# Kernel tuning notes

Measured on AMD Instinct MI355X. Metric: run time of the kernel, lower is better.

The kernel has to match this reference:

```python
import jax, jax.numpy as jnp
import numpy as np

N_NODES = 50000
N_EDGES = 1_250_000
D = 64
L = 3

def setup_inputs() -> dict:
    key = jax.random.key(0)
    k1, k2, k3, k4, k5, k6 = jax.random.split(key, 6)
    h = jax.random.normal(k1, (N_NODES, D), dtype=jnp.float32)
    edge_weight = jax.random.uniform(k2, (N_EDGES,), dtype=jnp.float32)
    # Glorot-ish scale keeps tanh in its responsive range
    Ws = jax.random.normal(k3, (L, D, D), dtype=jnp.float32) * (1.0 / np.sqrt(D))
    bs = jax.random.normal(k4, (L, D), dtype=jnp.float32) * 0.01
    src = jax.random.randint(k5, (N_EDGES,), 0, N_NODES, dtype=jnp.int64 if jax.config.jax_enable_x64 else jnp.int32)
    dst = jax.random.randint(k6, (N_EDGES,), 0, N_NODES, dtype=jnp.int64 if jax.config.jax_enable_x64 else jnp.int32)
    return {"h": h, "edge_weight": edge_weight, "Ws": Ws, "bs": bs, "src": src, "dst": dst}

def reference(h, edge_weight, Ws, bs, src, dst):
    # Stacked DGL GraphConv(norm='none'), edge-weighted: aggregate-then-transform
    # (in_feats == out_feats, so DGL aggregates first), tanh between layers,
    # concat of all intermediate representations along feature dim.
    n = h.shape[0]
    results = [h]
    for i in range(L):
        msg = h[src] * edge_weight[:, None]            # [E, D] gather-scale
        agg = jax.ops.segment_sum(msg, dst, num_segments=n)  # [N, D] scatter-add
        h = agg @ Ws[i] + bs[i]                        # dense transform + bias
        if i != L - 1:
            h = jnp.tanh(h)
        results.append(h)
    return jnp.concatenate(results, axis=1)           # [N, (L+1)*D]
```

## Files before the change

kernel.cpp:

```cpp
#include <hip/hip_runtime.h>
#include <hip/hip_fp16.h>
#include <math.h>

#define N_NODES 50000
#define N_EDGES 1250000
#define D 64
#define OUTC 256
#define CAP 64
#define SCAN_BLOCKS ((N_NODES + 255) / 256)

#define WSB_CNT      0
#define WSB_BUCKET   802816
#define WSB_H16_0    13602816
#define WSB_H16_1    20002816
#define WS_BUCKET_NEEDED 26402816

#define WS_DEG      0
#define WS_FILL     204800
#define WS_ROWPTR   409600
#define WS_BSUM     609664
#define WS_BOFF     610496
#define WS_EDGES    614400
#define WS_H16_0    10616832
#define WS_H16_1    (WS_H16_0 + (size_t)N_NODES * D * 2)
#define WS_F16_NEEDED (WS_H16_1 + (size_t)N_NODES * D * 2)
#define WS_CSR_NEEDED (WS_EDGES + (size_t)N_EDGES * 8)


#define PREP_T (50000 + 800000)
__global__ __launch_bounds__(256) void prep_kernel(const float* __restrict__ h,
                                                   float* __restrict__ out,
                                                   __half* __restrict__ h16,
                                                   int4* __restrict__ cnt4) {
    int tid = blockIdx.x * 256 + threadIdx.x;
    if (tid < 50000) { cnt4[tid] = make_int4(0, 0, 0, 0); return; }
    tid -= 50000;
    if (tid >= 800000) return;
    int row = tid >> 4;
    int c4  = tid & 15;
    float4 v = ((const float4*)h)[tid];
    ((float4*)(out + (size_t)row * OUTC))[c4] = v;
    __half2* p = (__half2*)(h16 + (size_t)row * D + c4 * 4);
    p[0] = __floats2half2_rn(v.x, v.y);
    p[1] = __floats2half2_rn(v.z, v.w);
}

#define FILL_GBLK 611
__global__ __launch_bounds__(256) void bucket_fill_kernel(const int* __restrict__ src,
                                                          const int* __restrict__ dst,
                                                          const float* __restrict__ ew,
                                                          int* __restrict__ cnt,
                                                          unsigned* __restrict__ bucket) {
    int p = blockIdx.x & 7;
    int g = blockIdx.x >> 3;
    int nlo = p * 6250, nhi = nlo + 6250;
    int e0 = (g * 256 + threadIdx.x) * 8;
    if (e0 >= N_EDGES) return;
    int4   d0 = *(const int4*)(dst + e0);
    int4   d1 = *(const int4*)(dst + e0 + 4);
    int4   s0 = *(const int4*)(src + e0);
    int4   s1 = *(const int4*)(src + e0 + 4);
    float4 w0 = *(const float4*)(ew + e0);
    float4 w1 = *(const float4*)(ew + e0 + 4);
    int   dd[8] = {d0.x, d0.y, d0.z, d0.w, d1.x, d1.y, d1.z, d1.w};
    int   ss[8] = {s0.x, s0.y, s0.z, s0.w, s1.x, s1.y, s1.z, s1.w};
    float ww[8] = {w0.x, w0.y, w0.z, w0.w, w1.x, w1.y, w1.z, w1.w};
#pragma unroll
    for (int i = 0; i < 8; i++) {
        int d = dd[i];
        if (d >= nlo && d < nhi) {
            int c = atomicAdd(&cnt[d * 4], 1) & (CAP - 1);
            unsigned hw = (unsigned)__half_as_ushort(__float2half(ww[i]));
            bucket[(size_t)d * CAP + c] = ((unsigned)ss[i] << 16) | hw;
        }
    }
}

#define LAYER5_BLOCKS 12500
__device__ __forceinline__ float rdlane(float v, int l) {
    return __int_as_float(__builtin_amdgcn_readlane(__float_as_int(v), l));
}
__global__ __launch_bounds__(256) void layer5_kernel(const __half* __restrict__ h16src,
                                                     const unsigned* __restrict__ bucket,
                                                     const int* __restrict__ cnt,
                                                     const float* __restrict__ W,
                                                     const float* __restrict__ bias,
                                                     float* __restrict__ hout,
                                                     __half* __restrict__ h16out,
                                                     int apply_tanh) {
    int t = threadIdx.x, lane = t & 63, wv = t >> 6;
    int fb = lane & 7;
    int eo = lane >> 3;
    const uint4* __restrict__ h4 = (const uint4*)h16src;
    float bv = bias[lane];

    int n  = __builtin_amdgcn_readfirstlane(blockIdx.x * 4 + wv);
    int cn = cnt[n * 4];
    const uint4* bp4 = (const uint4*)(bucket + (size_t)n * CAP);
    uint4 qqa = bp4[eo];
    cn = __builtin_amdgcn_readfirstlane(cn > CAP ? CAP : cn);
    int off2 = (cn > 32) ? 8 : 0;
    uint4 qqb = bp4[off2 + eo];

    float Wreg[D];
#pragma unroll
    for (int k = 0; k < D; k++) Wreg[k] = W[k * D + lane];

    float acc[8];
#pragma unroll
    for (int u = 0; u < 8; u++) acc[u] = 0.0f;

    auto processChunk = [&](uint4 qq, int j) {
        int sbase = j + eo * 4;
        unsigned ee[4];
        ee[0] = (sbase + 0 < cn) ? qq.x : 0u;
        ee[1] = (sbase + 1 < cn) ? qq.y : 0u;
        ee[2] = (sbase + 2 < cn) ? qq.z : 0u;
        ee[3] = (sbase + 3 < cn) ? qq.w : 0u;
        uint4 g[4];
#pragma unroll
        for (int i = 0; i < 4; i++)
            g[i] = h4[(size_t)(ee[i] >> 16) * 8 + fb];
#pragma unroll
        for (int i = 0; i < 4; i++) {
            float w = __half2float(__ushort_as_half((unsigned short)(ee[i] & 0xFFFFu)));
            const __half2* hv = (const __half2*)&g[i];
#pragma unroll
            for (int tt = 0; tt < 4; tt++) {
                float2 f = __half22float2(hv[tt]);
                acc[2 * tt]     = fmaf(f.x, w, acc[2 * tt]);
                acc[2 * tt + 1] = fmaf(f.y, w, acc[2 * tt + 1]);
            }
        }
    };

    processChunk(qqa, 0);
    if (cn > 32) processChunk(qqb, 32);

#pragma unroll
    for (int u = 0; u < 8; u++) {
        acc[u] += __shfl_xor(acc[u], 8);
        acc[u] += __shfl_xor(acc[u], 16);
        acc[u] += __shfl_xor(acc[u], 32);
    }

    float o0 = bv, o1 = 0.f, o2 = 0.f, o3 = 0.f;
#pragma unroll
    for (int k = 0; k < D; k += 4) {
        o0 = fmaf(rdlane(acc[(k + 0) & 7], (k + 0) >> 3), Wreg[k + 0], o0);
        o1 = fmaf(rdlane(acc[(k + 1) & 7], (k + 1) >> 3), Wreg[k + 1], o1);
        o2 = fmaf(rdlane(acc[(k + 2) & 7], (k + 2) >> 3), Wreg[k + 2], o2);
        o3 = fmaf(rdlane(acc[(k + 3) & 7], (k + 3) >> 3), Wreg[k + 3], o3);
    }
    float o = (o0 + o1) + (o2 + o3);
    if (apply_tanh) o = tanhf(o);
    hout[(size_t)n * OUTC + lane] = o;
    if (h16out) h16out[(size_t)n * D + lane] = __float2half(o);
}


__global__ __launch_bounds__(256) void copy_h_kernel(const float* __restrict__ h,
                                                     float* __restrict__ out,
                                                     __half* __restrict__ h16) {
    int idx = blockIdx.x * 256 + threadIdx.x;
    if (idx >= N_NODES * D / 4) return;
    int row = idx >> 4;
    int c4  = idx & 15;
    float4 v = ((const float4*)h)[idx];
    ((float4*)(out + (size_t)row * OUTC))[c4] = v;
    if (h16) {
        __half2* p = (__half2*)(h16 + (size_t)row * D + c4 * 4);
        p[0] = __floats2half2_rn(v.x, v.y);
        p[1] = __floats2half2_rn(v.z, v.w);
    }
}

__global__ __launch_bounds__(256) void hist_kernel(const int* __restrict__ dst,
                                                   int* __restrict__ deg) {
    int e = blockIdx.x * 256 + threadIdx.x;
    if (e >= N_EDGES) return;
    atomicAdd(&deg[dst[e]], 1);
}

__global__ __launch_bounds__(256) void scan_partial_kernel(const int* __restrict__ deg,
                                                           int* __restrict__ bsum) {
    __shared__ int ws4[4];
    int t = threadIdx.x;
    int i = blockIdx.x * 256 + t;
    int v = (i < N_NODES) ? deg[i] : 0;
#pragma unroll
    for (int off = 32; off >= 1; off >>= 1) v += __shfl_xor(v, off);
    if ((t & 63) == 0) ws4[t >> 6] = v;
    __syncthreads();
    if (t == 0) bsum[blockIdx.x] = ws4[0] + ws4[1] + ws4[2] + ws4[3];
}

__global__ __launch_bounds__(256) void scan_bsum_kernel(const int* __restrict__ bsum,
                                                        int* __restrict__ boff,
                                                        int* __restrict__ row_ptr) {
    __shared__ int wsum[4];
    int t = threadIdx.x, lane = t & 63, w = t >> 6;
    int v = (t < SCAN_BLOCKS) ? bsum[t] : 0;
    int x = v;
#pragma unroll
    for (int off = 1; off < 64; off <<= 1) {
        int y = __shfl_up(x, off);
        if (lane >= off) x += y;
    }
    if (lane == 63) wsum[w] = x;
    __syncthreads();
    int wo = 0;
    for (int u = 0; u < w; u++) wo += wsum[u];
    int excl = wo + x - v;
    if (t < SCAN_BLOCKS) boff[t] = excl;
    if (t == SCAN_BLOCKS - 1) row_ptr[N_NODES] = excl + v;
}

__global__ __launch_bounds__(256) void scan_final_kernel(const int* __restrict__ deg,
                                                         const int* __restrict__ boff,
                                                         int* __restrict__ row_ptr) {
    __shared__ int wsum[4];
    int t = threadIdx.x, lane = t & 63, w = t >> 6;
    int i = blockIdx.x * 256 + t;
    int v = (i < N_NODES) ? deg[i] : 0;
    int x = v;
#pragma unroll
    for (int off = 1; off < 64; off <<= 1) {
        int y = __shfl_up(x, off);
        if (lane >= off) x += y;
    }
    if (lane == 63) wsum[w] = x;
    __syncthreads();
    int wo = 0;
    for (int u = 0; u < w; u++) wo += wsum[u];
    if (i < N_NODES) row_ptr[i] = boff[blockIdx.x] + wo + (x - v);
}

__global__ __launch_bounds__(256) void fill_kernel(const int* __restrict__ src,
                                                   const int* __restrict__ dst,
                                                   const float* __restrict__ ew,
                                                   const int* __restrict__ row_ptr,
                                                   int* __restrict__ fill,
                                                   int2* __restrict__ edges) {
    int e = blockIdx.x * 256 + threadIdx.x;
    if (e >= N_EDGES) return;
    int d = dst[e];
    int p = atomicAdd(&fill[d], 1);
    edges[row_ptr[d] + p] = make_int2(src[e], __float_as_int(ew[e]));
}

#define LAYER_BLOCKS 3125
__global__ __launch_bounds__(256) void layer2_kernel(const __half* __restrict__ h16src,
                                                     const int2* __restrict__ edges,
                                                     const int* __restrict__ row_ptr,
                                                     const float* __restrict__ W,
                                                     const float* __restrict__ bias,
                                                     float* __restrict__ hout,
                                                     __half* __restrict__ h16out,
                                                     int apply_tanh) {
    __shared__ float Wlds[D * D];
    int t = threadIdx.x, lane = t & 63, wv = t >> 6;
    for (int i = t; i < D * D; i += 256) Wlds[i] = W[i];
    __syncthreads();
    int p  = lane & 31;
    int hh = lane >> 5;
    const __half2* __restrict__ h2 = (const __half2*)h16src;
    float bv = bias[lane];
    int waveId = blockIdx.x * 4 + wv;
    for (int n0 = waveId; n0 < N_NODES; n0 += LAYER_BLOCKS * 4) {
        int n = __builtin_amdgcn_readfirstlane(n0);
        int beg = __builtin_amdgcn_readfirstlane(row_ptr[n]);
        int end = __builtin_amdgcn_readfirstlane(row_ptr[n + 1]);
        float2 acc = make_float2(0.0f, 0.0f);
        int j = beg;
        for (; j + 8 <= end; j += 8) {
            int2 a0 = edges[j + 0], a1 = edges[j + 1];
            int2 a2 = edges[j + 2], a3 = edges[j + 3];
            int2 a4 = edges[j + 4], a5 = edges[j + 5];
            int2 a6 = edges[j + 6], a7 = edges[j + 7];
            int   s0 = hh ? a1.x : a0.x;  float w0 = __int_as_float(hh ? a1.y : a0.y);
            int   s1 = hh ? a3.x : a2.x;  float w1 = __int_as_float(hh ? a3.y : a2.y);
            int   s2 = hh ? a5.x : a4.x;  float w2 = __int_as_float(hh ? a5.y : a4.y);
            int   s3 = hh ? a7.x : a6.x;  float w3 = __int_as_float(hh ? a7.y : a6.y);
            __half2 v0 = h2[(size_t)s0 * 32 + p];
            __half2 v1 = h2[(size_t)s1 * 32 + p];
            __half2 v2 = h2[(size_t)s2 * 32 + p];
            __half2 v3 = h2[(size_t)s3 * 32 + p];
            acc.x = fmaf(__low2float(v0), w0, acc.x);  acc.y = fmaf(__high2float(v0), w0, acc.y);
            acc.x = fmaf(__low2float(v1), w1, acc.x);  acc.y = fmaf(__high2float(v1), w1, acc.y);
            acc.x = fmaf(__low2float(v2), w2, acc.x);  acc.y = fmaf(__high2float(v2), w2, acc.y);
            acc.x = fmaf(__low2float(v3), w3, acc.x);  acc.y = fmaf(__high2float(v3), w3, acc.y);
        }
        for (; j + 2 <= end; j += 2) {
            int2 a0 = edges[j], a1 = edges[j + 1];
            int   s0 = hh ? a1.x : a0.x;  float w0 = __int_as_float(hh ? a1.y : a0.y);
            __half2 v0 = h2[(size_t)s0 * 32 + p];
            acc.x = fmaf(__low2float(v0), w0, acc.x);  acc.y = fmaf(__high2float(v0), w0, acc.y);
        }
        if (j < end) {
            int2 a0 = edges[j];
            float w0 = hh ? 0.0f : __int_as_float(a0.y);
            __half2 v0 = h2[(size_t)a0.x * 32 + p];
            acc.x = fmaf(__low2float(v0), w0, acc.x);  acc.y = fmaf(__high2float(v0), w0, acc.y);
        }
        acc.x += __shfl_xor(acc.x, 32);
        acc.y += __shfl_xor(acc.y, 32);
        float o0 = bv, o1 = 0.f, o2 = 0.f, o3 = 0.f;
#pragma unroll
        for (int k = 0; k < D; k += 4) {
            int q = k >> 1;
            o0 = fmaf(__shfl(acc.x, q),     Wlds[(k + 0) * D + lane], o0);
            o1 = fmaf(__shfl(acc.y, q),     Wlds[(k + 1) * D + lane], o1);
            o2 = fmaf(__shfl(acc.x, q + 1), Wlds[(k + 2) * D + lane], o2);
            o3 = fmaf(__shfl(acc.y, q + 1), Wlds[(k + 3) * D + lane], o3);
        }
        float o = (o0 + o1) + (o2 + o3);
        if (apply_tanh) o = tanhf(o);
        hout[(size_t)n * OUTC + lane] = o;
        if (h16out) h16out[(size_t)n * D + lane] = __float2half(o);
    }
}

__global__ __launch_bounds__(256) void scatter_kernel(const float* __restrict__ hin,
                                                      const float* __restrict__ ew,
                                                      const int* __restrict__ src,
                                                      const int* __restrict__ dst,
                                                      float* __restrict__ agg) {
    long long gid = (long long)blockIdx.x * 256 + threadIdx.x;
    int e = (int)(gid >> 6);
    int lane = (int)(gid & 63);
    if (e >= N_EDGES) return;
    float v = hin[(size_t)src[e] * OUTC + lane] * ew[e];
    atomicAdd(&agg[(size_t)dst[e] * OUTC + lane], v);
}

__global__ __launch_bounds__(256) void gemm_kernel(float* __restrict__ hio,
                                                   const float* __restrict__ W,
                                                   const float* __restrict__ bias,
                                                   int apply_tanh) {
    __shared__ float Wl[D][D + 1];
    __shared__ float rowbuf[4][D];
    int t = threadIdx.x;
    for (int i = t; i < D * D; i += 256) Wl[i >> 6][i & (D - 1)] = W[i];
    int r = t >> 6, c = t & (D - 1);
    float bv = bias[c];
    int row0 = blockIdx.x * 64;
    for (int rr = 0; rr < 64; rr += 4) {
        int row = row0 + rr + r;
        __syncthreads();
        rowbuf[r][c] = (row < N_NODES) ? hio[(size_t)row * OUTC + c] : 0.0f;
        __syncthreads();
        float acc = bv;
#pragma unroll
        for (int k = 0; k < D; k++) acc = fmaf(rowbuf[r][k], Wl[k][c], acc);
        if (apply_tanh) acc = tanhf(acc);
        if (row < N_NODES) hio[(size_t)row * OUTC + c] = acc;
    }
}

extern "C" void kernel_launch(void* const* d_in, const int* in_sizes, int n_in,
                              void* d_out, int out_size, void* d_ws, size_t ws_size,
                              hipStream_t stream) {
    const float* h   = (const float*)d_in[0];
    const float* ew  = (const float*)d_in[1];
    const float* Ws  = (const float*)d_in[2];
    const float* bs  = (const float*)d_in[3];
    const int*   src = (const int*)d_in[4];
    const int*   dst = (const int*)d_in[5];
    float* out = (float*)d_out;

    if (ws_size >= WS_BUCKET_NEEDED) {
        char* ws = (char*)d_ws;
        int*      cnt    = (int*)(ws + WSB_CNT);
        unsigned* bucket = (unsigned*)(ws + WSB_BUCKET);
        __half*   h16a   = (__half*)(ws + WSB_H16_0);
        __half*   h16b   = (__half*)(ws + WSB_H16_1);

        prep_kernel<<<(PREP_T + 255) / 256, 256, 0, stream>>>(
            h, out, h16a, (int4*)cnt);
        bucket_fill_kernel<<<FILL_GBLK * 8, 256, 0, stream>>>(
            src, dst, ew, cnt, bucket);
        for (int i = 0; i < 3; i++) {
            float* hout = out + (size_t)(i + 1) * D;
            __half* hsrc = (i & 1) ? h16b : h16a;
            __half* hdst = (i == 2) ? nullptr : ((i & 1) ? h16a : h16b);
            layer5_kernel<<<LAYER5_BLOCKS, 256, 0, stream>>>(
                hsrc, bucket, cnt, Ws + (size_t)i * D * D, bs + (size_t)i * D,
                hout, hdst, (i < 2) ? 1 : 0);
        }
    } else if (ws_size >= WS_CSR_NEEDED) {
        char* ws = (char*)d_ws;
        int*  deg     = (int*)(ws + WS_DEG);
        int*  fillc   = (int*)(ws + WS_FILL);
        int*  row_ptr = (int*)(ws + WS_ROWPTR);
        int*  bsum    = (int*)(ws + WS_BSUM);
        int*  boff    = (int*)(ws + WS_BOFF);
        int2* edges   = (int2*)(ws + WS_EDGES);
        bool use_f16 = (ws_size >= WS_F16_NEEDED);
        __half* h16a = use_f16 ? (__half*)(ws + WS_H16_0) : nullptr;
        __half* h16b = use_f16 ? (__half*)(ws + WS_H16_1) : nullptr;

        hipMemsetAsync(ws, 0, WS_ROWPTR, stream);
        copy_h_kernel<<<(N_NODES * D / 4 + 255) / 256, 256, 0, stream>>>(h, out, h16a);
        hist_kernel<<<(N_EDGES + 255) / 256, 256, 0, stream>>>(dst, deg);
        scan_partial_kernel<<<SCAN_BLOCKS, 256, 0, stream>>>(deg, bsum);
        scan_bsum_kernel<<<1, 256, 0, stream>>>(bsum, boff, row_ptr);
        scan_final_kernel<<<SCAN_BLOCKS, 256, 0, stream>>>(deg, boff, row_ptr);
        fill_kernel<<<(N_EDGES + 255) / 256, 256, 0, stream>>>(src, dst, ew, row_ptr, fillc, edges);
        for (int i = 0; i < 3; i++) {
            float* hout = out + (size_t)(i + 1) * D;
            __half* hsrc = (i & 1) ? h16b : h16a;
            __half* hdst = (i == 2) ? nullptr : ((i & 1) ? h16a : h16b);
            layer2_kernel<<<LAYER_BLOCKS, 256, 0, stream>>>(
                hsrc, edges, row_ptr, Ws + (size_t)i * D * D, bs + (size_t)i * D,
                hout, hdst, (i < 2) ? 1 : 0);
        }
    } else {
        hipMemsetAsync(out, 0, (size_t)N_NODES * OUTC * sizeof(float), stream);
        copy_h_kernel<<<(N_NODES * D / 4 + 255) / 256, 256, 0, stream>>>(h, out, nullptr);
        for (int i = 0; i < 3; i++) {
            const float* hin = out + (size_t)i * D;
            float*       agg = out + (size_t)(i + 1) * D;
            long long nthreads = (long long)N_EDGES * 64;
            scatter_kernel<<<(int)((nthreads + 255) / 256), 256, 0, stream>>>(hin, ew, src, dst, agg);
            gemm_kernel<<<(N_NODES + 63) / 64, 256, 0, stream>>>(
                agg, Ws + (size_t)i * D * D, bs + (size_t)i * D, (i < 2) ? 1 : 0);
        }
    }
}
```

Before: 260.0 us.

## Reorder to transform-then-aggregate with separate GEMM kernel and reduce-scatter shuffle

Splits each layer into a dense per-node W multiply written in place to the fp16 feature buffer, followed by an aggregation kernel that gathers the already-transformed rows and adds bias/tanh. It also replaces the butterfly all-reduce plus 64 readlane dot product with a reduce-scatter shuffle pattern, so each lane ends with one output feature. The intent is to remove the per-node W register load and per-node matvec from the latency-bound gather kernel. In exchange it adds an extra kernel launch and an extra read/write pass over node features per layer, and it rounds to fp16 an additional time after the transform.

```diff
diff --git a/kernel.cpp b/kernel.cpp
--- a/kernel.cpp
+++ b/kernel.cpp
@@ -76,23 +76,43 @@
     }
 }
 
-#define LAYER5_BLOCKS 12500
-__device__ __forceinline__ float rdlane(float v, int l) {
-    return __int_as_float(__builtin_amdgcn_readlane(__float_as_int(v), l));
-}
-__global__ __launch_bounds__(256) void layer5_kernel(const __half* __restrict__ h16src,
-                                                     const unsigned* __restrict__ bucket,
-                                                     const int* __restrict__ cnt,
-                                                     const float* __restrict__ W,
-                                                     const float* __restrict__ bias,
-                                                     float* __restrict__ hout,
-                                                     __half* __restrict__ h16out,
-                                                     int apply_tanh) {
+
+#define WGEMM_BLOCKS 782
+__global__ __launch_bounds__(256) void wgemm_kernel(__half* __restrict__ xy,
+                                                    const float* __restrict__ W) {
+    int t = threadIdx.x, lane = t & 63, wv = t >> 6;
+    float Wreg[D];
+#pragma unroll
+    for (int k = 0; k < D; k++) Wreg[k] = W[k * D + lane];
+    int row0 = blockIdx.x * 64 + wv * 16;
+#pragma unroll 1
+    for (int r = 0; r < 16; r++) {
+        int row = row0 + r;
+        if (row >= N_NODES) break;
+        const __half2* __restrict__ xr = (const __half2*)(xy + (size_t)row * D);
+        float o = 0.0f;
+#pragma unroll
+        for (int j = 0; j < 32; j++) {
+            float2 x2 = __half22float2(xr[j]);
+            o = fmaf(x2.x, Wreg[2 * j],     o);
+            o = fmaf(x2.y, Wreg[2 * j + 1], o);
+        }
+        xy[(size_t)row * D + lane] = __float2half(o);
+    }
+}
+
+#define AGG_BLOCKS 12500
+__global__ __launch_bounds__(256) void agg_kernel(const __half* __restrict__ y16,
+                                                  const unsigned* __restrict__ bucket,
+                                                  const int* __restrict__ cnt,
+                                                  const float* __restrict__ bias,
+                                                  float* __restrict__ hout,
+                                                  __half* __restrict__ h16out,
+                                                  int apply_tanh) {
     int t = threadIdx.x, lane = t & 63, wv = t >> 6;
     int fb = lane & 7;
     int eo = lane >> 3;
-    const uint4* __restrict__ h4 = (const uint4*)h16src;
-    float bv = bias[lane];
+    const uint4* __restrict__ h4 = (const uint4*)y16;
 
     int n  = __builtin_amdgcn_readfirstlane(blockIdx.x * 4 + wv);
     int cn = cnt[n * 4];
@@ -101,10 +121,6 @@
     cn = __builtin_amdgcn_readfirstlane(cn > CAP ? CAP : cn);
     int off2 = (cn > 32) ? 8 : 0;
     uint4 qqb = bp4[off2 + eo];
-
-    float Wreg[D];
-#pragma unroll
-    for (int k = 0; k < D; k++) Wreg[k] = W[k * D + lane];
 
     float acc[8];
 #pragma unroll
@@ -127,9 +143,9 @@
             const __half2* hv = (const __half2*)&g[i];
 #pragma unroll
             for (int tt = 0; tt < 4; tt++) {
-                float2 f = __half22float2(hv[tt]);
-                acc[2 * tt]     = fmaf(f.x, w, acc[2 * tt]);
-                acc[2 * tt + 1] = fmaf(f.y, w, acc[2 * tt + 1]);
+                float2 f2 = __half22float2(hv[tt]);
+                acc[2 * tt]     = fmaf(f2.x, w, acc[2 * tt]);
+                acc[2 * tt + 1] = fmaf(f2.y, w, acc[2 * tt + 1]);
             }
         }
     };
@@ -137,25 +153,30 @@
     processChunk(qqa, 0);
     if (cn > 32) processChunk(qqb, 32);
 
-#pragma unroll
-    for (int u = 0; u < 8; u++) {
-        acc[u] += __shfl_xor(acc[u], 8);
-        acc[u] += __shfl_xor(acc[u], 16);
-        acc[u] += __shfl_xor(acc[u], 32);
-    }
-
-    float o0 = bv, o1 = 0.f, o2 = 0.f, o3 = 0.f;
-#pragma unroll
-    for (int k = 0; k < D; k += 4) {
-        o0 = fmaf(rdlane(acc[(k + 0) & 7], (k + 0) >> 3), Wreg[k + 0], o0);
-        o1 = fmaf(rdlane(acc[(k + 1) & 7], (k + 1) >> 3), Wreg[k + 1], o1);
-        o2 = fmaf(rdlane(acc[(k + 2) & 7], (k + 2) >> 3), Wreg[k + 2], o2);
-        o3 = fmaf(rdlane(acc[(k + 3) & 7], (k + 3) >> 3), Wreg[k + 3], o3);
-    }
-    float o = (o0 + o1) + (o2 + o3);
+    int b0 = (lane >> 3) & 1, b1 = (lane >> 4) & 1, b2 = (lane >> 5) & 1;
+    float k1[4];
+#pragma unroll
+    for (int j = 0; j < 4; j++) {
+        float send = b0 ? acc[2 * j] : acc[2 * j + 1];
+        float keep = b0 ? acc[2 * j + 1] : acc[2 * j];
+        k1[j] = keep + __shfl_xor(send, 8);
+    }
+    float k2[2];
+#pragma unroll
+    for (int j = 0; j < 2; j++) {
+        float send = b1 ? k1[2 * j] : k1[2 * j + 1];
+        float keep = b1 ? k1[2 * j + 1] : k1[2 * j];
+        k2[j] = keep + __shfl_xor(send, 16);
+    }
+    float send = b2 ? k2[0] : k2[1];
+    float keep = b2 ? k2[1] : k2[0];
+    float o = keep + __shfl_xor(send, 32);
+
+    int f = (fb << 3) | eo;
+    o += bias[f];
     if (apply_tanh) o = tanhf(o);
-    hout[(size_t)n * OUTC + lane] = o;
-    if (h16out) h16out[(size_t)n * D + lane] = __float2half(o);
+    hout[(size_t)n * OUTC + f] = o;
+    if (h16out) h16out[(size_t)n * D + f] = __float2half(o);
 }
 
 
@@ -380,13 +401,15 @@
             h, out, h16a, (int4*)cnt);
         bucket_fill_kernel<<<FILL_GBLK * 8, 256, 0, stream>>>(
             src, dst, ew, cnt, bucket);
+        __half* cur = h16a;
+        __half* nxt = h16b;
         for (int i = 0; i < 3; i++) {
-            float* hout = out + (size_t)(i + 1) * D;
-            __half* hsrc = (i & 1) ? h16b : h16a;
-            __half* hdst = (i == 2) ? nullptr : ((i & 1) ? h16a : h16b);
-            layer5_kernel<<<LAYER5_BLOCKS, 256, 0, stream>>>(
-                hsrc, bucket, cnt, Ws + (size_t)i * D * D, bs + (size_t)i * D,
-                hout, hdst, (i < 2) ? 1 : 0);
+            wgemm_kernel<<<WGEMM_BLOCKS, 256, 0, stream>>>(cur, Ws + (size_t)i * D * D);
+            agg_kernel<<<AGG_BLOCKS, 256, 0, stream>>>(
+                cur, bucket, cnt, bs + (size_t)i * D,
+                out + (size_t)(i + 1) * D,
+                (i == 2) ? nullptr : nxt, (i < 2) ? 1 : 0);
+            __half* tmp = cur; cur = nxt; nxt = tmp;
         }
     } else if (ws_size >= WS_CSR_NEEDED) {
         char* ws = (char*)d_ws;
```

Result: slower. 273.7 us (+5.3%).

## Fuse bucket fill with input copy, stage W in LDS, use reduce-scatter shuffles

Applied to the files above, without the earlier changes.

The bucket-fill and the h copy/fp16 conversion now run as one kernel, and the counter zeroing moves to a hipMemsetAsync, so one launch disappears and the two independent jobs can overlap. The layer kernel stages W transposed in padded shared memory instead of holding 64 floats per thread in registers. It also issues both gather chunks before accumulating, and replaces the butterfly all-reduce with a reduce-scatter that leaves one feature per lane. This should lower register pressure and shuffle count and raise occupancy and memory-level parallelism, at the cost of a per-block W load into LDS plus a __syncthreads.

```diff
diff --git a/kernel.cpp b/kernel.cpp
--- a/kernel.cpp
+++ b/kernel.cpp
@@ -27,60 +27,58 @@
 #define WS_CSR_NEEDED (WS_EDGES + (size_t)N_EDGES * 8)
 
 
-#define PREP_T (50000 + 800000)
-__global__ __launch_bounds__(256) void prep_kernel(const float* __restrict__ h,
-                                                   float* __restrict__ out,
-                                                   __half* __restrict__ h16,
-                                                   int4* __restrict__ cnt4) {
-    int tid = blockIdx.x * 256 + threadIdx.x;
-    if (tid < 50000) { cnt4[tid] = make_int4(0, 0, 0, 0); return; }
-    tid -= 50000;
-    if (tid >= 800000) return;
-    int row = tid >> 4;
-    int c4  = tid & 15;
-    float4 v = ((const float4*)h)[tid];
-    ((float4*)(out + (size_t)row * OUTC))[c4] = v;
-    __half2* p = (__half2*)(h16 + (size_t)row * D + c4 * 4);
-    p[0] = __floats2half2_rn(v.x, v.y);
-    p[1] = __floats2half2_rn(v.z, v.w);
-}
-
-#define FILL_GBLK 611
-__global__ __launch_bounds__(256) void bucket_fill_kernel(const int* __restrict__ src,
-                                                          const int* __restrict__ dst,
-                                                          const float* __restrict__ ew,
-                                                          int* __restrict__ cnt,
-                                                          unsigned* __restrict__ bucket) {
-    int p = blockIdx.x & 7;
-    int g = blockIdx.x >> 3;
-    int nlo = p * 6250, nhi = nlo + 6250;
-    int e0 = (g * 256 + threadIdx.x) * 8;
-    if (e0 >= N_EDGES) return;
-    int4   d0 = *(const int4*)(dst + e0);
-    int4   d1 = *(const int4*)(dst + e0 + 4);
-    int4   s0 = *(const int4*)(src + e0);
-    int4   s1 = *(const int4*)(src + e0 + 4);
-    float4 w0 = *(const float4*)(ew + e0);
-    float4 w1 = *(const float4*)(ew + e0 + 4);
-    int   dd[8] = {d0.x, d0.y, d0.z, d0.w, d1.x, d1.y, d1.z, d1.w};
-    int   ss[8] = {s0.x, s0.y, s0.z, s0.w, s1.x, s1.y, s1.z, s1.w};
-    float ww[8] = {w0.x, w0.y, w0.z, w0.w, w1.x, w1.y, w1.z, w1.w};
-#pragma unroll
-    for (int i = 0; i < 8; i++) {
-        int d = dd[i];
-        if (d >= nlo && d < nhi) {
-            int c = atomicAdd(&cnt[d * 4], 1) & (CAP - 1);
-            unsigned hw = (unsigned)__half_as_ushort(__float2half(ww[i]));
-            bucket[(size_t)d * CAP + c] = ((unsigned)ss[i] << 16) | hw;
-        }
-    }
-}
-
-#define LAYER5_BLOCKS 12500
+#define FILLCOPY_FILLB 4888
+#define FILLCOPY_COPYB 3125
+__global__ __launch_bounds__(256) void fillcopy_kernel(const int* __restrict__ src,
+                                                       const int* __restrict__ dst,
+                                                       const float* __restrict__ ew,
+                                                       int* __restrict__ cnt,
+                                                       unsigned* __restrict__ bucket,
+                                                       const float* __restrict__ h,
+                                                       float* __restrict__ out,
+                                                       __half* __restrict__ h16) {
+    if (blockIdx.x < FILLCOPY_FILLB) {
+        int p = blockIdx.x & 7;
+        int g = blockIdx.x >> 3;
+        int nlo = p * 6250, nhi = nlo + 6250;
+        int e0 = (g * 256 + threadIdx.x) * 8;
+        if (e0 >= N_EDGES) return;
+        int4   d0 = *(const int4*)(dst + e0);
+        int4   d1 = *(const int4*)(dst + e0 + 4);
+        int4   s0 = *(const int4*)(src + e0);
+        int4   s1 = *(const int4*)(src + e0 + 4);
+        float4 w0 = *(const float4*)(ew + e0);
+        float4 w1 = *(const float4*)(ew + e0 + 4);
+        int   dd[8] = {d0.x, d0.y, d0.z, d0.w, d1.x, d1.y, d1.z, d1.w};
+        int   ss[8] = {s0.x, s0.y, s0.z, s0.w, s1.x, s1.y, s1.z, s1.w};
+        float ww[8] = {w0.x, w0.y, w0.z, w0.w, w1.x, w1.y, w1.z, w1.w};
+#pragma unroll
+        for (int i = 0; i < 8; i++) {
+            int d = dd[i];
+            if (d >= nlo && d < nhi) {
+                int c = atomicAdd(&cnt[d * 4], 1) & (CAP - 1);
+                unsigned hw = (unsigned)__half_as_ushort(__float2half(ww[i]));
+                bucket[(size_t)d * CAP + c] = ((unsigned)ss[i] << 16) | hw;
+            }
+        }
+    } else {
+        int tid = (blockIdx.x - FILLCOPY_FILLB) * 256 + threadIdx.x;
+        if (tid >= 800000) return;
+        int row = tid >> 4;
+        int c4  = tid & 15;
+        float4 v = ((const float4*)h)[tid];
+        ((float4*)(out + (size_t)row * OUTC))[c4] = v;
+        __half2* pp = (__half2*)(h16 + (size_t)row * D + c4 * 4);
+        pp[0] = __floats2half2_rn(v.x, v.y);
+        pp[1] = __floats2half2_rn(v.z, v.w);
+    }
+}
+
+#define LAYER7_BLOCKS 12500
 __device__ __forceinline__ float rdlane(float v, int l) {
     return __int_as_float(__builtin_amdgcn_readlane(__float_as_int(v), l));
 }
-__global__ __launch_bounds__(256) void layer5_kernel(const __half* __restrict__ h16src,
+__global__ __launch_bounds__(256) void layer7_kernel(const __half* __restrict__ h16src,
                                                      const unsigned* __restrict__ bucket,
                                                      const int* __restrict__ cnt,
                                                      const float* __restrict__ W,
@@ -88,69 +86,107 @@
                                                      float* __restrict__ hout,
                                                      __half* __restrict__ h16out,
                                                      int apply_tanh) {
+    __shared__ float Wt[D * 68];
     int t = threadIdx.x, lane = t & 63, wv = t >> 6;
     int fb = lane & 7;
     int eo = lane >> 3;
     const uint4* __restrict__ h4 = (const uint4*)h16src;
-    float bv = bias[lane];
-
-    int n  = __builtin_amdgcn_readfirstlane(blockIdx.x * 4 + wv);
-    int cn = cnt[n * 4];
+
+    int n = __builtin_amdgcn_readfirstlane(blockIdx.x * 4 + wv);
+    int cn_raw = cnt[n * 4];
     const uint4* bp4 = (const uint4*)(bucket + (size_t)n * CAP);
     uint4 qqa = bp4[eo];
-    cn = __builtin_amdgcn_readfirstlane(cn > CAP ? CAP : cn);
-    int off2 = (cn > 32) ? 8 : 0;
-    uint4 qqb = bp4[off2 + eo];
-
-    float Wreg[D];
-#pragma unroll
-    for (int k = 0; k < D; k++) Wreg[k] = W[k * D + lane];
+    float bv = bias[lane];
+
+#pragma unroll
+    for (int i = t; i < D * D; i += 256)
+        Wt[(i & 63) * 68 + (i >> 6)] = W[i];
+
+    int cn = __builtin_amdgcn_readfirstlane(cn_raw > CAP ? CAP : cn_raw);
+    int hasB = (cn > 32);
+    uint4 qqb = bp4[(hasB ? 8 : 0) + eo];
+    __syncthreads();
 
     float acc[8];
 #pragma unroll
     for (int u = 0; u < 8; u++) acc[u] = 0.0f;
 
-    auto processChunk = [&](uint4 qq, int j) {
-        int sbase = j + eo * 4;
-        unsigned ee[4];
-        ee[0] = (sbase + 0 < cn) ? qq.x : 0u;
-        ee[1] = (sbase + 1 < cn) ? qq.y : 0u;
-        ee[2] = (sbase + 2 < cn) ? qq.z : 0u;
-        ee[3] = (sbase + 3 < cn) ? qq.w : 0u;
-        uint4 g[4];
+    unsigned eeA[4], eeB[4];
+    uint4 gA[4], gB[4];
+    {
+        int sb = eo * 4;
+        eeA[0] = (sb + 0 < cn) ? qqa.x : 0u;
+        eeA[1] = (sb + 1 < cn) ? qqa.y : 0u;
+        eeA[2] = (sb + 2 < cn) ? qqa.z : 0u;
+        eeA[3] = (sb + 3 < cn) ? qqa.w : 0u;
 #pragma unroll
         for (int i = 0; i < 4; i++)
-            g[i] = h4[(size_t)(ee[i] >> 16) * 8 + fb];
+            gA[i] = h4[(size_t)(eeA[i] >> 16) * 8 + fb];
+    }
+    if (hasB) {
+        int sb = 32 + eo * 4;
+        eeB[0] = (sb + 0 < cn) ? qqb.x : 0u;
+        eeB[1] = (sb + 1 < cn) ? qqb.y : 0u;
+        eeB[2] = (sb + 2 < cn) ? qqb.z : 0u;
+        eeB[3] = (sb + 3 < cn) ? qqb.w : 0u;
+#pragma unroll
+        for (int i = 0; i < 4; i++)
+            gB[i] = h4[(size_t)(eeB[i] >> 16) * 8 + fb];
+    }
+#pragma unroll
+    for (int i = 0; i < 4; i++) {
+        float w = __half2float(__ushort_as_half((unsigned short)(eeA[i] & 0xFFFFu)));
+        const __half2* hv = (const __half2*)&gA[i];
+#pragma unroll
+        for (int tt = 0; tt < 4; tt++) {
+            float2 f2 = __half22float2(hv[tt]);
+            acc[2 * tt]     = fmaf(f2.x, w, acc[2 * tt]);
+            acc[2 * tt + 1] = fmaf(f2.y, w, acc[2 * tt + 1]);
+        }
+    }
+    if (hasB) {
 #pragma unroll
         for (int i = 0; i < 4; i++) {
-            float w = __half2float(__ushort_as_half((unsigned short)(ee[i] & 0xFFFFu)));
-            const __half2* hv = (const __half2*)&g[i];
+            float w = __half2float(__ushort_as_half((unsigned short)(eeB[i] & 0xFFFFu)));
+            const __half2* hv = (const __half2*)&gB[i];
 #pragma unroll
             for (int tt = 0; tt < 4; tt++) {
-                float2 f = __half22float2(hv[tt]);
-                acc[2 * tt]     = fmaf(f.x, w, acc[2 * tt]);
-                acc[2 * tt + 1] = fmaf(f.y, w, acc[2 * tt + 1]);
+                float2 f2 = __half22float2(hv[tt]);
+                acc[2 * tt]     = fmaf(f2.x, w, acc[2 * tt]);
+                acc[2 * tt + 1] = fmaf(f2.y, w, acc[2 * tt + 1]);
             }
         }
-    };
-
-    processChunk(qqa, 0);
-    if (cn > 32) processChunk(qqb, 32);
-
-#pragma unroll
-    for (int u = 0; u < 8; u++) {
-        acc[u] += __shfl_xor(acc[u], 8);
-        acc[u] += __shfl_xor(acc[u], 16);
-        acc[u] += __shfl_xor(acc[u], 32);
-    }
-
+    }
+
+    int b0 = (lane >> 3) & 1, b1 = (lane >> 4) & 1, b2 = (lane >> 5) & 1;
+    float k1[4];
+#pragma unroll
+    for (int j = 0; j < 4; j++) {
+        float send = b0 ? acc[2 * j] : acc[2 * j + 1];
+        float keep = b0 ? acc[2 * j + 1] : acc[2 * j];
+        k1[j] = keep + __shfl_xor(send, 8);
+    }
+    float k2[2];
+#pragma unroll
+    for (int j = 0; j < 2; j++) {
+        float send = b1 ? k1[2 * j] : k1[2 * j + 1];
+        float keep = b1 ? k1[2 * j + 1] : k1[2 * j];
+        k2[j] = keep + __shfl_xor(send, 16);
+    }
+    float send = b2 ? k2[0] : k2[1];
+    float keep = b2 ? k2[1] : k2[0];
+    float a_scat = keep + __shfl_xor(send, 32);
+
+    const float4* wcol = (const float4*)&Wt[lane * 68];
     float o0 = bv, o1 = 0.f, o2 = 0.f, o3 = 0.f;
 #pragma unroll
-    for (int k = 0; k < D; k += 4) {
-        o0 = fmaf(rdlane(acc[(k + 0) & 7], (k + 0) >> 3), Wreg[k + 0], o0);
-        o1 = fmaf(rdlane(acc[(k + 1) & 7], (k + 1) >> 3), Wreg[k + 1], o1);
-        o2 = fmaf(rdlane(acc[(k + 2) & 7], (k + 2) >> 3), Wreg[k + 2], o2);
-        o3 = fmaf(rdlane(acc[(k + 3) & 7], (k + 3) >> 3), Wreg[k + 3], o3);
+    for (int tq = 0; tq < 16; tq++) {
+        float4 wq = wcol[tq];
+        int k = tq * 4;
+        o0 = fmaf(rdlane(a_scat, (((k + 0) & 7) << 3) | ((k + 0) >> 3)), wq.x, o0);
+        o1 = fmaf(rdlane(a_scat, (((k + 1) & 7) << 3) | ((k + 1) >> 3)), wq.y, o1);
+        o2 = fmaf(rdlane(a_scat, (((k + 2) & 7) << 3) | ((k + 2) >> 3)), wq.z, o2);
+        o3 = fmaf(rdlane(a_scat, (((k + 3) & 7) << 3) | ((k + 3) >> 3)), wq.w, o3);
     }
     float o = (o0 + o1) + (o2 + o3);
     if (apply_tanh) o = tanhf(o);
@@ -376,15 +412,14 @@
         __half*   h16a   = (__half*)(ws + WSB_H16_0);
         __half*   h16b   = (__half*)(ws + WSB_H16_1);
 
-        prep_kernel<<<(PREP_T + 255) / 256, 256, 0, stream>>>(
-            h, out, h16a, (int4*)cnt);
-        bucket_fill_kernel<<<FILL_GBLK * 8, 256, 0, stream>>>(
-            src, dst, ew, cnt, bucket);
+        hipMemsetAsync(cnt, 0, 800000, stream);
+        fillcopy_kernel<<<FILLCOPY_FILLB + FILLCOPY_COPYB, 256, 0, stream>>>(
+            src, dst, ew, cnt, bucket, h, out, h16a);
         for (int i = 0; i < 3; i++) {
             float* hout = out + (size_t)(i + 1) * D;
             __half* hsrc = (i & 1) ? h16b : h16a;
             __half* hdst = (i == 2) ? nullptr : ((i & 1) ? h16a : h16b);
-            layer5_kernel<<<LAYER5_BLOCKS, 256, 0, stream>>>(
+            layer7_kernel<<<LAYER7_BLOCKS, 256, 0, stream>>>(
                 hsrc, bucket, cnt, Ws + (size_t)i * D * D, bs + (size_t)i * D,
                 hout, hdst, (i < 2) ? 1 : 0);
         }
```

New measurement: 248.0 us. -4.6%, faster.
